# Kernel optimization log

Hardware: AMD Instinct MI355X
Metric: run time of the kernel (lower is better)

## Reference

```python
import jax, jax.numpy as jnp
import numpy as np

N = 8192          # number of nodes
IN_F = 256        # in_features
OUT_F = 128       # out_features
ALPHA = 0.2       # LeakyReLU negative slope


def setup_inputs() -> dict:
    key = jax.random.key(0)
    k1, k2, k3, k4 = jax.random.split(key, 4)
    h = jax.random.normal(k1, (N, IN_F), dtype=jnp.float32)
    adj = jax.random.randint(k2, (N, N), 0, 2, dtype=jnp.int32)  # dense 0/1 adjacency mask
    W = (jax.random.normal(k3, (IN_F, OUT_F), dtype=jnp.float32) * 0.05)   # W.weight^T
    a = (jax.random.normal(k4, (2 * OUT_F,), dtype=jnp.float32) * 0.05)    # a.weight flattened
    return {"h": h, "adj": adj, "W": W, "a": a}


def reference(h, adj, W, a):
    # Wh = self.W(h): [N, OUT_F]
    Wh = h @ W
    # Original builds an [N, N, 2F] concat tensor then projects with 'a'.
    # Equivalent math: e[i, j] = leaky_relu(Wh[i]@a1 + Wh[j]@a2)
    a1, a2 = a[:OUT_F], a[OUT_F:]
    src = Wh @ a1                                     # [N] per-source score
    dst = Wh @ a2                                     # [N] per-target score
    e = jax.nn.leaky_relu(src[:, None] + dst[None, :], negative_slope=ALPHA)  # [N, N]
    # masked softmax over neighbors (dim=1); adj==0 -> -inf
    e = jnp.where(adj == 0, -jnp.inf, e)
    attention = jax.nn.softmax(e, axis=1)             # [N, N]
    # dropout p=0 in eval-mode reference -> identity
    h_prime = attention @ Wh                          # [N, OUT_F]
    return jax.nn.elu(h_prime)                        # concat=True -> ELU
```

## Files before the change

kernel.cpp:

```cpp
#include <hip/hip_runtime.h>
#include <math.h>

#define N 8192
#define IN_F 256
#define OUT_F 128
#define ALPHA 0.2f

typedef _Float16 f16;
typedef __attribute__((ext_vector_type(4))) float f32x4;
typedef __attribute__((ext_vector_type(8))) _Float16 f16x8;
typedef __attribute__((ext_vector_type(4))) _Float16 f16x4;

__global__ __launch_bounds__(256) void k_prep(const float* __restrict__ W,
                                              f16* __restrict__ WT) {
    int idx = blockIdx.x * 256 + threadIdx.x;
    int f = idx >> 8;
    int k = idx & 255;
    WT[idx] = (f16)W[k * OUT_F + f];
}

#define HS 280
__global__ __launch_bounds__(256) void k_wh(const float* __restrict__ h,
                                            const f16* __restrict__ WT,
                                            const float* __restrict__ a,
                                            f16* __restrict__ WhT,
                                            float* __restrict__ src,
                                            float* __restrict__ dst) {
    __shared__ __align__(16) f16 hA[32][HS];
    __shared__ __align__(16) f16 outT[128][40];
    __shared__ float sred[4][32], dred[4][32];

    const int t = threadIdx.x;
    const int i0 = blockIdx.x * 32;
    const int wv = t >> 6, l = t & 63, ln = l & 15, lq = l >> 4;

    {
        const float4* hg = (const float4*)(h + (size_t)i0 * IN_F);
#pragma unroll
        for (int it = 0; it < 8; ++it) {
            int idx = t + it * 256;
            int r = idx >> 6;
            int c4 = (idx & 63) * 4;
            float4 v = hg[idx];
            f16x4 p = { (f16)v.x, (f16)v.y, (f16)v.z, (f16)v.w };
            *(f16x4*)&hA[r][c4] = p;
        }
    }
    __syncthreads();

    f32x4 acc00 = {0.f,0.f,0.f,0.f}, acc01 = {0.f,0.f,0.f,0.f};
    f32x4 acc10 = {0.f,0.f,0.f,0.f}, acc11 = {0.f,0.f,0.f,0.f};
    const int f0 = 32 * wv;

#pragma unroll
    for (int ks = 0; ks < 8; ++ks) {
        const int k0 = 32 * ks + 8 * lq;
        f16x8 a0 = *(const f16x8*)&hA[ln][k0];
        f16x8 a1 = *(const f16x8*)&hA[16 + ln][k0];
        f16x8 b0 = *(const f16x8*)(WT + (size_t)(f0 + ln) * IN_F + k0);
        f16x8 b1 = *(const f16x8*)(WT + (size_t)(f0 + 16 + ln) * IN_F + k0);
        acc00 = __builtin_amdgcn_mfma_f32_16x16x32_f16(a0, b0, acc00, 0, 0, 0);
        acc01 = __builtin_amdgcn_mfma_f32_16x16x32_f16(a0, b1, acc01, 0, 0, 0);
        acc10 = __builtin_amdgcn_mfma_f32_16x16x32_f16(a1, b0, acc10, 0, 0, 0);
        acc11 = __builtin_amdgcn_mfma_f32_16x16x32_f16(a1, b1, acc11, 0, 0, 0);
    }

    const float a1c0 = a[f0 + ln],      a2c0 = a[128 + f0 + ln];
    const float a1c1 = a[f0 + 16 + ln], a2c1 = a[128 + f0 + 16 + ln];
    float sp[8], dp[8];
#pragma unroll
    for (int i = 0; i < 8; ++i) { sp[i] = 0.f; dp[i] = 0.f; }

#pragma unroll
    for (int hh = 0; hh < 2; ++hh) {
        f32x4 v0 = hh ? acc10 : acc00;
        f32x4 v1 = hh ? acc11 : acc01;
        f16x4 p0, p1;
#pragma unroll
        for (int rg = 0; rg < 4; ++rg) {
            sp[hh * 4 + rg] += v0[rg] * a1c0 + v1[rg] * a1c1;
            dp[hh * 4 + rg] += v0[rg] * a2c0 + v1[rg] * a2c1;
            p0[rg] = (f16)v0[rg];
            p1[rg] = (f16)v1[rg];
        }
        *(f16x4*)&outT[f0 + ln][16 * hh + 4 * lq] = p0;
        *(f16x4*)&outT[f0 + 16 + ln][16 * hh + 4 * lq] = p1;
    }
#pragma unroll
    for (int i = 0; i < 8; ++i) {
        float s = sp[i], d = dp[i];
        s += __shfl_down(s, 8, 16); d += __shfl_down(d, 8, 16);
        s += __shfl_down(s, 4, 16); d += __shfl_down(d, 4, 16);
        s += __shfl_down(s, 2, 16); d += __shfl_down(d, 2, 16);
        s += __shfl_down(s, 1, 16); d += __shfl_down(d, 1, 16);
        if (ln == 0) {
            int row = 16 * (i >> 2) + 4 * lq + (i & 3);
            sred[wv][row] = s;
            dred[wv][row] = d;
        }
    }
    __syncthreads();
    if (t < 32) {
        src[i0 + t] = sred[0][t] + sred[1][t] + sred[2][t] + sred[3][t];
        dst[i0 + t] = dred[0][t] + dred[1][t] + dred[2][t] + dred[3][t];
    }
    {
        const int col = t & 127, g = t >> 7;
        f16x8 q0 = *(const f16x8*)&outT[col][16 * g];
        f16x8 q1 = *(const f16x8*)&outT[col][16 * g + 8];
        *(f16x8*)(WhT + (size_t)col * N + i0 + 16 * g) = q0;
        *(f16x8*)(WhT + (size_t)col * N + i0 + 16 * g + 8) = q1;
    }
}

#define TI 32
#define NJ 128
#define NC (N / NJ)
#define WSTRIDE 152
__global__ __launch_bounds__(512) void k_attn(const int* __restrict__ adj,
                                              const f16* __restrict__ WhT,
                                              const float* __restrict__ src,
                                              const float* __restrict__ dst,
                                              float* __restrict__ out) {
    __shared__ __align__(16) f16 wA[2][TI][WSTRIDE];
    __shared__ float lfin[TI];

    const int t = threadIdx.x;
    const int i0 = blockIdx.x * TI;
    const int pr = t >> 4;
    const int pm = t & 15;
    const int wv = t >> 6;
    const int l = t & 63, ln = l & 15, lq = l >> 4;

    const float my_src = src[i0 + pr];
    const float cshift = fabsf(my_src) + 4.0f;
    float lp = 0.f;
    f32x4 accv0 = {0.f,0.f,0.f,0.f}, accv1 = {0.f,0.f,0.f,0.f};

    const int* arow = adj + (size_t)(i0 + pr) * N;
    const f16* Bb = WhT + (size_t)(16 * wv + ln) * N + 8 * lq;

    int4 aA0, aB0, aA1, aB1;
    float4 dA0, dB0, dA1, dB1;

    auto issue = [&](int c, int4& xA, int4& xB, float4& xdA, float4& xdB) {
        const int j0 = c * NJ + 8 * pm;
        xA = *(const int4*)(arow + j0);
        xB = *(const int4*)(arow + j0 + 4);
        xdA = *(const float4*)(dst + j0);
        xdB = *(const float4*)(dst + j0 + 4);
    };
    auto produce = [&](int c, const int4& xA, const int4& xB,
                       const float4& xdA, const float4& xdB) {
        float w[8];
        const int*   av = (const int*)&xA;
        const int*   bv = (const int*)&xB;
        const float* df = (const float*)&xdA;
        const float* ef = (const float*)&xdB;
#pragma unroll
        for (int k = 0; k < 4; ++k) {
            float e = my_src + df[k];
            float lk = e > 0.f ? e : ALPHA * e;
            w[k] = av[k] ? __expf(lk - cshift) : 0.f;
        }
#pragma unroll
        for (int k = 0; k < 4; ++k) {
            float e = my_src + ef[k];
            float lk = e > 0.f ? e : ALPHA * e;
            w[4 + k] = bv[k] ? __expf(lk - cshift) : 0.f;
        }
        f16x8 wp;
#pragma unroll
        for (int k = 0; k < 8; ++k) { lp += w[k]; wp[k] = (f16)w[k]; }
        *(f16x8*)&wA[c & 1][pr][8 * pm] = wp;
    };
    auto mpass = [&](int c) {
        const f16* wb = &wA[c & 1][0][0];
        const f16* bp = Bb + c * NJ;
#pragma unroll
        for (int ks = 0; ks < 4; ++ks) {
            const int k0 = 32 * ks;
            f16x8 bf = *(const f16x8*)(bp + k0);
            f16x8 a0 = *(const f16x8*)(wb + ln * WSTRIDE + k0 + 8 * lq);
            f16x8 a1 = *(const f16x8*)(wb + (16 + ln) * WSTRIDE + k0 + 8 * lq);
            accv0 = __builtin_amdgcn_mfma_f32_16x16x32_f16(a0, bf, accv0, 0, 0, 0);
            accv1 = __builtin_amdgcn_mfma_f32_16x16x32_f16(a1, bf, accv1, 0, 0, 0);
        }
    };

    issue(0, aA0, aB0, dA0, dB0);
    produce(0, aA0, aB0, dA0, dB0);
    issue(1, aA1, aB1, dA1, dB1);
    __syncthreads();

    for (int cc = 0; cc < NC; cc += 2) {
        if (cc + 2 < NC) issue(cc + 2, aA0, aB0, dA0, dB0);
        mpass(cc);
        produce(cc + 1, aA1, aB1, dA1, dB1);
        __syncthreads();
        if (cc + 3 < NC) issue(cc + 3, aA1, aB1, dA1, dB1);
        mpass(cc + 1);
        if (cc + 2 < NC) produce(cc + 2, aA0, aB0, dA0, dB0);
        __syncthreads();
    }

    {
        float v = lp;
        v += __shfl_down(v, 8, 16);
        v += __shfl_down(v, 4, 16);
        v += __shfl_down(v, 2, 16);
        v += __shfl_down(v, 1, 16);
        if (pm == 0) lfin[pr] = v;
    }
    __syncthreads();

#pragma unroll
    for (int hh = 0; hh < 2; ++hh) {
        f32x4 av = hh ? accv1 : accv0;
#pragma unroll
        for (int rg = 0; rg < 4; ++rg) {
            const int row = 16 * hh + 4 * lq + rg;
            float hp = av[rg] / lfin[row];
            float res = hp > 0.f ? hp : expm1f(hp);
            out[(size_t)(i0 + row) * OUT_F + 16 * wv + ln] = res;
        }
    }
}

extern "C" void kernel_launch(void* const* d_in, const int* in_sizes, int n_in,
                              void* d_out, int out_size, void* d_ws, size_t ws_size,
                              hipStream_t stream) {
    const float* h   = (const float*)d_in[0];
    const int*   adj = (const int*)d_in[1];
    const float* W   = (const float*)d_in[2];
    const float* a   = (const float*)d_in[3];
    float* out = (float*)d_out;

    f16*   WT  = (f16*)d_ws;
    f16*   WhT = (f16*)((char*)d_ws + (1 << 16));
    float* src = (float*)((char*)WhT + (size_t)OUT_F * N * sizeof(f16));
    float* dst = src + N;

    k_prep<<<128, 256, 0, stream>>>(W, WT);
    k_wh<<<N / 32, 256, 0, stream>>>(h, WT, a, WhT, src, dst);
    k_attn<<<N / TI, 512, 0, stream>>>(adj, WhT, src, dst, out);
}
```

Before: 417.7 us.

## Split attention over neighbor halves with partial sums and a combine kernel

```diff
diff --git a/kernel.cpp b/kernel.cpp
--- a/kernel.cpp
+++ b/kernel.cpp
@@ -106,27 +106,32 @@
     }
     {
         const int col = t & 127, g = t >> 7;
+        const int ct = i0 >> 7, jo = i0 & 127;
         f16x8 q0 = *(const f16x8*)&outT[col][16 * g];
         f16x8 q1 = *(const f16x8*)&outT[col][16 * g + 8];
-        *(f16x8*)(WhT + (size_t)col * N + i0 + 16 * g) = q0;
-        *(f16x8*)(WhT + (size_t)col * N + i0 + 16 * g + 8) = q1;
-    }
-}
-
-#define TI 32
+        f16* dstp = WhT + (size_t)ct * (128 * 128) + (size_t)col * 128 + jo + 16 * g;
+        *(f16x8*)(dstp) = q0;
+        *(f16x8*)(dstp + 8) = q1;
+    }
+}
+
+#define TI 16
 #define NJ 128
-#define NC (N / NJ)
+#define JS 2
+#define NCL (N / NJ / JS)
 #define WSTRIDE 152
-__global__ __launch_bounds__(512) void k_attn(const int* __restrict__ adj,
-                                              const f16* __restrict__ WhT,
-                                              const float* __restrict__ src,
-                                              const float* __restrict__ dst,
-                                              float* __restrict__ out) {
+__global__ __launch_bounds__(256, 4) void k_attn(const int* __restrict__ adj,
+                                                 const f16* __restrict__ WhT,
+                                                 const float* __restrict__ src,
+                                                 const float* __restrict__ dst,
+                                                 float* __restrict__ p_part,
+                                                 float* __restrict__ l_part) {
     __shared__ __align__(16) f16 wA[2][TI][WSTRIDE];
     __shared__ float lfin[TI];
 
     const int t = threadIdx.x;
     const int i0 = blockIdx.x * TI;
+    const int jh = blockIdx.y;
     const int pr = t >> 4;
     const int pm = t & 15;
     const int wv = t >> 6;
@@ -137,18 +142,20 @@
     float lp = 0.f;
     f32x4 accv0 = {0.f,0.f,0.f,0.f}, accv1 = {0.f,0.f,0.f,0.f};
 
-    const int* arow = adj + (size_t)(i0 + pr) * N;
-    const f16* Bb = WhT + (size_t)(16 * wv + ln) * N + 8 * lq;
+    const int* arow = adj + (size_t)(i0 + pr) * N + jh * (N / JS) + 8 * pm;
+    const float* drow = dst + jh * (N / JS) + 8 * pm;
+    const f16* Bb = WhT + (size_t)(jh * NCL) * (128 * 128)
+                  + (size_t)(32 * wv + ln) * 128 + 8 * lq;
 
     int4 aA0, aB0, aA1, aB1;
     float4 dA0, dB0, dA1, dB1;
 
     auto issue = [&](int c, int4& xA, int4& xB, float4& xdA, float4& xdB) {
-        const int j0 = c * NJ + 8 * pm;
+        const int j0 = c * NJ;
         xA = *(const int4*)(arow + j0);
         xB = *(const int4*)(arow + j0 + 4);
-        xdA = *(const float4*)(dst + j0);
-        xdB = *(const float4*)(dst + j0 + 4);
+        xdA = *(const float4*)(drow + j0);
+        xdB = *(const float4*)(drow + j0 + 4);
     };
     auto produce = [&](int c, const int4& xA, const int4& xB,
                        const float4& xdA, const float4& xdB) {
@@ -176,15 +183,15 @@
     };
     auto mpass = [&](int c) {
         const f16* wb = &wA[c & 1][0][0];
-        const f16* bp = Bb + c * NJ;
+        const f16* bp = Bb + (size_t)c * (128 * 128);
 #pragma unroll
         for (int ks = 0; ks < 4; ++ks) {
             const int k0 = 32 * ks;
-            f16x8 bf = *(const f16x8*)(bp + k0);
             f16x8 a0 = *(const f16x8*)(wb + ln * WSTRIDE + k0 + 8 * lq);
-            f16x8 a1 = *(const f16x8*)(wb + (16 + ln) * WSTRIDE + k0 + 8 * lq);
-            accv0 = __builtin_amdgcn_mfma_f32_16x16x32_f16(a0, bf, accv0, 0, 0, 0);
-            accv1 = __builtin_amdgcn_mfma_f32_16x16x32_f16(a1, bf, accv1, 0, 0, 0);
+            f16x8 b0 = *(const f16x8*)(bp + k0);
+            f16x8 b1 = *(const f16x8*)(bp + 16 * 128 + k0);
+            accv0 = __builtin_amdgcn_mfma_f32_16x16x32_f16(a0, b0, accv0, 0, 0, 0);
+            accv1 = __builtin_amdgcn_mfma_f32_16x16x32_f16(a0, b1, accv1, 0, 0, 0);
         }
     };
 
@@ -193,14 +200,14 @@
     issue(1, aA1, aB1, dA1, dB1);
     __syncthreads();
 
-    for (int cc = 0; cc < NC; cc += 2) {
-        if (cc + 2 < NC) issue(cc + 2, aA0, aB0, dA0, dB0);
+    for (int cc = 0; cc < NCL; cc += 2) {
+        if (cc + 2 < NCL) issue(cc + 2, aA0, aB0, dA0, dB0);
         mpass(cc);
         produce(cc + 1, aA1, aB1, dA1, dB1);
         __syncthreads();
-        if (cc + 3 < NC) issue(cc + 3, aA1, aB1, dA1, dB1);
+        if (cc + 3 < NCL) issue(cc + 3, aA1, aB1, dA1, dB1);
         mpass(cc + 1);
-        if (cc + 2 < NC) produce(cc + 2, aA0, aB0, dA0, dB0);
+        if (cc + 2 < NCL) produce(cc + 2, aA0, aB0, dA0, dB0);
         __syncthreads();
     }
 
@@ -213,18 +220,29 @@
         if (pm == 0) lfin[pr] = v;
     }
     __syncthreads();
-
+    if (t < TI) l_part[(size_t)jh * N + i0 + t] = lfin[t];
+
+    float* pb = p_part + (size_t)jh * N * OUT_F;
 #pragma unroll
     for (int hh = 0; hh < 2; ++hh) {
         f32x4 av = hh ? accv1 : accv0;
 #pragma unroll
         for (int rg = 0; rg < 4; ++rg) {
-            const int row = 16 * hh + 4 * lq + rg;
-            float hp = av[rg] / lfin[row];
-            float res = hp > 0.f ? hp : expm1f(hp);
-            out[(size_t)(i0 + row) * OUT_F + 16 * wv + ln] = res;
-        }
-    }
+            const int row = 4 * lq + rg;
+            pb[(size_t)(i0 + row) * OUT_F + 32 * wv + 16 * hh + ln] = av[rg];
+        }
+    }
+}
+
+__global__ __launch_bounds__(256) void k_comb(const float* __restrict__ p_part,
+                                              const float* __restrict__ l_part,
+                                              float* __restrict__ out) {
+    const int idx = blockIdx.x * 256 + threadIdx.x;
+    const int row = idx >> 7;
+    float p = p_part[idx] + p_part[(size_t)N * OUT_F + idx];
+    float lsum = l_part[row] + l_part[N + row];
+    float hp = p / lsum;
+    out[idx] = hp > 0.f ? hp : expm1f(hp);
 }
 
 extern "C" void kernel_launch(void* const* d_in, const int* in_sizes, int n_in,
@@ -236,12 +254,17 @@
     const float* a   = (const float*)d_in[3];
     float* out = (float*)d_out;
 
-    f16*   WT  = (f16*)d_ws;
-    f16*   WhT = (f16*)((char*)d_ws + (1 << 16));
-    float* src = (float*)((char*)WhT + (size_t)OUT_F * N * sizeof(f16));
-    float* dst = src + N;
+    char* ws = (char*)d_ws;
+    f16*   WT     = (f16*)ws;                       ws += 64 * 1024;
+    f16*   WhT    = (f16*)ws;                       ws += 2 * 1024 * 1024;
+    float* src    = (float*)ws;                     ws += N * sizeof(float);
+    float* dst    = (float*)ws;                     ws += N * sizeof(float);
+    float* l_part = (float*)ws;                     ws += JS * N * sizeof(float);
+    float* p_part = (float*)ws;
 
     k_prep<<<128, 256, 0, stream>>>(W, WT);
     k_wh<<<N / 32, 256, 0, stream>>>(h, WT, a, WhT, src, dst);
-    k_attn<<<N / TI, 512, 0, stream>>>(adj, WhT, src, dst, out);
-}
+    dim3 agrid(N / TI, JS);
+    k_attn<<<agrid, 256, 0, stream>>>(adj, WhT, src, dst, p_part, l_part);
+    k_comb<<<N * OUT_F / 256, 256, 0, stream>>>(p_part, l_part, out);
+}
```

Result: slower. 450.1 us (+7.8%).
